# Performance work log

Hardware: AMD Instinct MI355X
Metric: run time of the kernel (lower is better)

## Reference

```python
import jax, jax.numpy as jnp
import numpy as np
from jax import lax

DN = ('NCHW', 'OIHW', 'NCHW')
N_LEVELS = 5


def conv(x, w, b=None, stride=1):
    y = lax.conv_general_dilated(x, w, (stride, stride), 'VALID', dimension_numbers=DN)
    if b is not None:
        y = y + b.reshape(1, -1, 1, 1)
    return y


def conv3_replicate(x, w, b):
    # 3x3 conv, padding=1, padding_mode='replicate'
    xp = jnp.pad(x, ((0, 0), (0, 0), (1, 1), (1, 1)), mode='edge')
    return conv(xp, w, b)


def conv_transpose3_s2(x, w):
    # ConvTranspose2d(k=3, stride=2, padding=0): n -> 2n+1
    return lax.conv_general_dilated(x, jnp.flip(w, (2, 3)), (1, 1), [(2, 2), (2, 2)],
                                    lhs_dilation=(2, 2), dimension_numbers=DN)


def setup_inputs() -> dict:
    key = jax.random.key(0)
    ks = jax.random.split(key, 12)
    B = 1024
    u = jax.random.normal(ks[0], (B, 1, 127, 127), jnp.float32)
    f = jax.random.normal(ks[1], (B, 1, 127, 127), jnp.float32)
    a = jax.random.uniform(ks[2], (B, 1, 128, 128), jnp.float32)
    s = 0.3
    c0_w = jax.random.normal(ks[3], (N_LEVELS, 1, 1, 3, 3), jnp.float32) * s  # Conv_Dyn.conv_0
    c0_b = jax.random.normal(ks[4], (N_LEVELS, 1), jnp.float32) * s
    c1_w = jax.random.normal(ks[5], (N_LEVELS, 1, 1, 2, 2), jnp.float32) * s  # Conv_Dyn.conv_1
    c1_b = jax.random.normal(ks[6], (N_LEVELS, 1), jnp.float32) * s
    r1_w = jax.random.normal(ks[7], (N_LEVELS - 1, 1, 1, 2, 2), jnp.float32) * s  # MgRestriction.R_1
    r3_w = jax.random.normal(ks[8], (N_LEVELS - 1, 1, 1, 3, 3), jnp.float32) * s  # MgRestriction.R_3
    t_w = jax.random.normal(ks[9], (N_LEVELS - 1, 1, 1, 3, 3), jnp.float32) * s  # transpose_layers
    return dict(u=u, f=f, a=a, c0_w=c0_w, c0_b=c0_b, c1_w=c1_w, c1_b=c1_b,
                r1_w=r1_w, r3_w=r3_w, t_w=t_w)


def reference(u, f, a, c0_w, c0_b, c1_w, c1_b, r1_w, r3_w, t_w):
    a_top = a
    # level 0: Conv_Dyn with u given, diva None
    diva = conv(a, c1_w[0], c1_b[0])                 # [B,1,127,127]
    r = f - diva * u
    u_lvl = u + conv3_replicate(jnp.tanh(diva), c0_w[0], c0_b[0]) * r
    diva_list = [diva]
    us = [u_lvl]
    # levels 1..4: restriction then Conv_Dyn (u=None branch, f=None so r kept)
    for i in range(1, N_LEVELS):
        a = conv(a, r1_w[i - 1], stride=2)           # R_1: k2 s2
        r = conv(r, r3_w[i - 1], stride=2)           # R_3: k3 s2
        diva = conv(a, c1_w[i], c1_b[i])
        u_lvl = conv3_replicate(jnp.tanh(diva), c0_w[i], c0_b[i]) * r
        diva_list.append(diva)
        us.append(u_lvl)
    # prolongation: coarse-to-fine residual additions
    for i in range(N_LEVELS - 2, -1, -1):
        us[i] = us[i] + conv_transpose3_s2(us[i + 1], t_w[i])
    return (us[0], f, a_top, *diva_list)
```

## Files before the change

kernel.cpp:

```cpp
#include <hip/hip_runtime.h>
#include <cmath>

#define BATCH 1024

__global__ __launch_bounds__(256) void k_L01(
    const float* __restrict__ u, const float* __restrict__ f, const float* __restrict__ a,
    const float* __restrict__ c0w, const float* __restrict__ c0b,
    const float* __restrict__ c1w, const float* __restrict__ c1b,
    const float* __restrict__ r1w, const float* __restrict__ r3w,
    float* __restrict__ out_us0, float* __restrict__ out_diva0,
    float* __restrict__ out_f, float* __restrict__ out_a,
    float* __restrict__ out_diva1,
    float* __restrict__ ws_a1, float* __restrict__ ws_r1, float* __restrict__ ws_us1)
{
    const int b = blockIdx.y;
    const int bx = blockIdx.x;
    const int Y0 = bx * 16;
    const int y0 = bx * 8;
    const int tid = threadIdx.x;

    __shared__ float asrc[22][128];
    __shared__ float td0[18][128];
    __shared__ float r0s[17][128];
    __shared__ float a1s[11][66];
    __shared__ float td1[10][64];

    const float* ab = a + (size_t)b * 16384;
    for (int i = tid; i < 22 * 128; i += 256) {
        int r = i >> 7, c = i & 127;
        int g = Y0 - 2 + r; g = g < 0 ? 0 : (g > 127 ? 127 : g);
        asrc[r][c] = ab[g * 128 + c];
    }
    __syncthreads();

    const float w00 = c1w[0], w01 = c1w[1], w10 = c1w[2], w11 = c1w[3], b1 = c1b[0];
    for (int i = tid; i < 18 * 127; i += 256) {
        int r = i / 127, c = i % 127;
        int g = Y0 - 1 + r;
        if (g >= 0 && g <= 126) {
            float d = asrc[r + 1][c] * w00 + asrc[r + 1][c + 1] * w01
                    + asrc[r + 2][c] * w10 + asrc[r + 2][c + 1] * w11 + b1;
            td0[r][c] = tanhf(d);
        }
    }
    __syncthreads();

    {
        float* oa = out_a + (size_t)b * 16384 + (size_t)Y0 * 128;
        for (int i = tid; i < 16 * 128; i += 256)
            oa[i] = asrc[(i >> 7) + 2][i & 127];
    }

    const float c0b0 = c0b[0];
    for (int i = tid; i < 17 * 127; i += 256) {
        int rr = i / 127, c = i % 127;
        int g = Y0 + rr;
        if (g > 126) continue;
        float diva = asrc[rr + 2][c] * w00 + asrc[rr + 2][c + 1] * w01
                   + asrc[rr + 3][c] * w10 + asrc[rr + 3][c + 1] * w11 + b1;
        size_t idx = (size_t)b * 16129 + (size_t)g * 127 + c;
        float uv = u[idx], fv = f[idx];
        float rv = fv - diva * uv;
        r0s[rr][c] = rv;
        if (rr < 16) {
            float s = c0b0;
            #pragma unroll
            for (int ky = 0; ky < 3; ky++) {
                int sy = g - 1 + ky; sy = sy < 0 ? 0 : (sy > 126 ? 126 : sy);
                int lr = sy - (Y0 - 1);
                #pragma unroll
                for (int kx = 0; kx < 3; kx++) {
                    int sx = c - 1 + kx; sx = sx < 0 ? 0 : (sx > 126 ? 126 : sx);
                    s += c0w[ky * 3 + kx] * td0[lr][sx];
                }
            }
            out_diva0[idx] = diva;
            out_us0[idx] = uv + s * rv;
            out_f[idx] = fv;
        }
    }

    const float q00 = r1w[0], q01 = r1w[1], q10 = r1w[2], q11 = r1w[3];
    for (int i = tid; i < 11 * 66; i += 256) {
        int rA = i / 66, cA = i % 66;
        int ay = y0 - 1 + rA; ay = ay < 0 ? 0 : (ay > 63 ? 63 : ay);
        int ax = cA - 1; ax = ax < 0 ? 0 : (ax > 63 ? 63 : ax);
        int la = 2 * ay - Y0 + 2;
        a1s[rA][cA] = asrc[la][2 * ax] * q00 + asrc[la][2 * ax + 1] * q01
                    + asrc[la + 1][2 * ax] * q10 + asrc[la + 1][2 * ax + 1] * q11;
    }
    __syncthreads();

    {
        float* a1o = ws_a1 + (size_t)b * 4096 + (size_t)y0 * 64;
        for (int i = tid; i < 8 * 64; i += 256)
            a1o[i] = a1s[(i >> 6) + 1][(i & 63) + 1];
    }

    const float v00 = c1w[4], v01 = c1w[5], v10 = c1w[6], v11 = c1w[7], b2 = c1b[1];
    for (int i = tid; i < 10 * 63; i += 256) {
        int rt = i / 63, c = i % 63;
        int dy = y0 - 1 + rt;
        if (dy >= 0 && dy <= 62) {
            float d = a1s[rt][c + 1] * v00 + a1s[rt][c + 2] * v01
                    + a1s[rt + 1][c + 1] * v10 + a1s[rt + 1][c + 2] * v11 + b2;
            td1[rt][c] = tanhf(d);
        }
    }
    __syncthreads();

    const float c0b1 = c0b[1];
    const float* c0w1 = c0w + 9;
    const float* r3 = r3w;
    for (int i = tid; i < 8 * 63; i += 256) {
        int row = i / 63, col = i % 63;
        int y = y0 + row;
        if (y > 62) continue;
        float diva = a1s[row + 1][col + 1] * v00 + a1s[row + 1][col + 2] * v01
                   + a1s[row + 2][col + 1] * v10 + a1s[row + 2][col + 2] * v11 + b2;
        float rv = 0.f;
        #pragma unroll
        for (int p = 0; p < 3; p++)
            #pragma unroll
            for (int q = 0; q < 3; q++)
                rv += r3[p * 3 + q] * r0s[2 * row + p][2 * col + q];
        float s = c0b1;
        #pragma unroll
        for (int ky = 0; ky < 3; ky++) {
            int sy = y - 1 + ky; sy = sy < 0 ? 0 : (sy > 62 ? 62 : sy);
            int lr = sy - (y0 - 1);
            #pragma unroll
            for (int kx = 0; kx < 3; kx++) {
                int sx = col - 1 + kx; sx = sx < 0 ? 0 : (sx > 62 ? 62 : sx);
                s += c0w1[ky * 3 + kx] * td1[lr][sx];
            }
        }
        size_t idx = (size_t)b * 3969 + (size_t)y * 63 + col;
        out_diva1[idx] = diva;
        ws_r1[idx] = rv;
        ws_us1[idx] = s * rv;
    }
}

template<int N, int NA, int PA, int PD>
__device__ __forceinline__ void level_step(
    const float* ap, const float* rp, float* ac, float* rc, float* us, float* td,
    const float* __restrict__ r1w, const float* __restrict__ r3w,
    const float* __restrict__ c1w, float c1b_,
    const float* __restrict__ c0w, float c0b_,
    float* __restrict__ diva_out, int tid)
{
    const float q00 = r1w[0], q01 = r1w[1], q10 = r1w[2], q11 = r1w[3];
    for (int idx = tid; idx < NA * NA; idx += 256) {
        int y = idx / NA, x = idx % NA;
        const float* p = ap + 2 * y * PA + 2 * x;
        ac[idx] = p[0] * q00 + p[1] * q01 + p[PA] * q10 + p[PA + 1] * q11;
    }
    __syncthreads();
    const float w00 = c1w[0], w01 = c1w[1], w10 = c1w[2], w11 = c1w[3];
    for (int idx = tid; idx < N * N; idx += 256) {
        int y = idx / N, x = idx % N;
        float d = ac[y * NA + x] * w00 + ac[y * NA + x + 1] * w01
                + ac[(y + 1) * NA + x] * w10 + ac[(y + 1) * NA + x + 1] * w11 + c1b_;
        td[idx] = tanhf(d);
        diva_out[idx] = d;
    }
    __syncthreads();
    for (int idx = tid; idx < N * N; idx += 256) {
        int y = idx / N, x = idx % N;
        float rv = 0.f;
        #pragma unroll
        for (int p = 0; p < 3; p++)
            #pragma unroll
            for (int q = 0; q < 3; q++)
                rv += r3w[p * 3 + q] * rp[(2 * y + p) * PD + 2 * x + q];
        float s = c0b_;
        #pragma unroll
        for (int ky = 0; ky < 3; ky++) {
            int sy = y - 1 + ky; sy = sy < 0 ? 0 : (sy > N - 1 ? N - 1 : sy);
            #pragma unroll
            for (int kx = 0; kx < 3; kx++) {
                int sx = x - 1 + kx; sx = sx < 0 ? 0 : (sx > N - 1 ? N - 1 : sx);
                s += c0w[ky * 3 + kx] * td[sy * N + sx];
            }
        }
        rc[idx] = rv;
        us[idx] = s * rv;
    }
    __syncthreads();
}

template<int NO, int NI>
__device__ __forceinline__ void prolong_step(
    float* uo, const float* ui, const float* __restrict__ tw9, int tid)
{
    for (int idx = tid; idx < NO * NO; idx += 256) {
        int y = idx / NO, x = idx % NO;
        float acc = 0.f;
        #pragma unroll
        for (int ky = 0; ky < 3; ky++) {
            int sy = y - ky;
            if (sy & 1) continue;
            int iy = sy >> 1;
            if (iy < 0 || iy >= NI) continue;
            #pragma unroll
            for (int kx = 0; kx < 3; kx++) {
                int sx = x - kx;
                if (sx & 1) continue;
                int ix = sx >> 1;
                if (ix < 0 || ix >= NI) continue;
                acc += tw9[ky * 3 + kx] * ui[iy * NI + ix];
            }
        }
        uo[idx] += acc;
    }
    __syncthreads();
}

__global__ __launch_bounds__(256) void k_coarse(
    const float* __restrict__ a1, const float* __restrict__ r1,
    const float* __restrict__ r1w, const float* __restrict__ r3w,
    const float* __restrict__ c1w, const float* __restrict__ c1b,
    const float* __restrict__ c0w, const float* __restrict__ c0b,
    const float* __restrict__ tw,
    float* __restrict__ diva2, float* __restrict__ diva3, float* __restrict__ diva4,
    float* __restrict__ us2_out)
{
    const int b = blockIdx.x;
    const int tid = threadIdx.x;
    __shared__ float aA[64 * 64];
    __shared__ float rA[63 * 63];
    __shared__ float aB[32 * 32];
    __shared__ float rB[31 * 31];
    __shared__ float aC[16 * 16];
    __shared__ float rC[15 * 15];
    __shared__ float aD[8 * 8];
    __shared__ float rD[7 * 7];
    __shared__ float us2s[31 * 31];
    __shared__ float us3s[15 * 15];
    __shared__ float us4s[7 * 7];
    __shared__ float td[31 * 31];

    const float* a1b = a1 + (size_t)b * 4096;
    const float* r1b = r1 + (size_t)b * 3969;
    for (int i = tid; i < 4096; i += 256) aA[i] = a1b[i];
    for (int i = tid; i < 3969; i += 256) rA[i] = r1b[i];
    __syncthreads();

    level_step<31, 32, 64, 63>(aA, rA, aB, rB, us2s, td,
        r1w + 4, r3w + 9, c1w + 8, c1b[2], c0w + 18, c0b[2],
        diva2 + (size_t)b * 961, tid);
    level_step<15, 16, 32, 31>(aB, rB, aC, rC, us3s, td,
        r1w + 8, r3w + 18, c1w + 12, c1b[3], c0w + 27, c0b[3],
        diva3 + (size_t)b * 225, tid);
    level_step<7, 8, 16, 15>(aC, rC, aD, rD, us4s, td,
        r1w + 12, r3w + 27, c1w + 16, c1b[4], c0w + 36, c0b[4],
        diva4 + (size_t)b * 49, tid);

    prolong_step<15, 7>(us3s, us4s, tw + 27, tid);
    prolong_step<31, 15>(us2s, us3s, tw + 18, tid);

    for (int i = tid; i < 961; i += 256)
        us2_out[(size_t)b * 961 + i] = us2s[i];
}

__global__ __launch_bounds__(256) void k_prolong2(
    float* __restrict__ us0, const float* __restrict__ us1, const float* __restrict__ us2,
    const float* __restrict__ tw)
{
    const int b = blockIdx.y;
    const int bx = blockIdx.x;
    const int Y0 = bx * 16;
    const int y0 = bx * 8;
    const int tid = threadIdx.x;
    __shared__ float us2s[6][32];
    __shared__ float us1p[9][64];

    const float* i2 = us2 + (size_t)b * 961;
    for (int i = tid; i < 6 * 31; i += 256) {
        int r = i / 31, c = i % 31;
        int jy = 4 * bx - 2 + r;
        if (jy >= 0 && jy <= 30) us2s[r][c] = i2[jy * 31 + c];
    }
    __syncthreads();

    const float* t1 = tw + 9;
    const float* i1 = us1 + (size_t)b * 3969;
    for (int i = tid; i < 9 * 63; i += 256) {
        int r = i / 63, c = i % 63;
        int iy = y0 - 1 + r;
        if (iy < 0 || iy > 62) continue;
        float acc = i1[iy * 63 + c];
        #pragma unroll
        for (int ky = 0; ky < 3; ky++) {
            int sy = iy - ky;
            if ((sy & 1) || sy < 0) continue;
            int jy = sy >> 1;
            if (jy > 30) continue;
            int lr = jy - (4 * bx - 2);
            #pragma unroll
            for (int kx = 0; kx < 3; kx++) {
                int sx = c - kx;
                if ((sx & 1) || sx < 0) continue;
                int jx = sx >> 1;
                if (jx > 30) continue;
                acc += t1[ky * 3 + kx] * us2s[lr][jx];
            }
        }
        us1p[r][c] = acc;
    }
    __syncthreads();

    const float* t0 = tw;
    float* o0 = us0 + (size_t)b * 16129;
    for (int i = tid; i < 16 * 127; i += 256) {
        int row = i / 127, col = i % 127;
        int y = Y0 + row;
        if (y > 126) continue;
        float acc = 0.f;
        #pragma unroll
        for (int ky = 0; ky < 3; ky++) {
            int sy = y - ky;
            if ((sy & 1) || sy < 0) continue;
            int iy = sy >> 1;
            if (iy > 62) continue;
            int lr = iy - (y0 - 1);
            #pragma unroll
            for (int kx = 0; kx < 3; kx++) {
                int sx = col - kx;
                if ((sx & 1) || sx < 0) continue;
                int ix = sx >> 1;
                if (ix > 62) continue;
                acc += t0[ky * 3 + kx] * us1p[lr][ix];
            }
        }
        o0[(size_t)y * 127 + col] += acc;
    }
}

extern "C" void kernel_launch(void* const* d_in, const int* in_sizes, int n_in,
                              void* d_out, int out_size, void* d_ws, size_t ws_size,
                              hipStream_t stream) {
    const float* u   = (const float*)d_in[0];
    const float* f   = (const float*)d_in[1];
    const float* a   = (const float*)d_in[2];
    const float* c0w = (const float*)d_in[3];
    const float* c0b = (const float*)d_in[4];
    const float* c1w = (const float*)d_in[5];
    const float* c1b = (const float*)d_in[6];
    const float* r1w = (const float*)d_in[7];
    const float* r3w = (const float*)d_in[8];
    const float* tw  = (const float*)d_in[9];
    float* out = (float*)d_out;
    float* ws  = (float*)d_ws;
    const size_t B = BATCH;

    size_t off_us0 = 0;
    size_t off_f   = B * 16129;
    size_t off_a   = off_f + B * 16129;
    size_t off_d0  = off_a + B * 16384;
    size_t off_d1  = off_d0 + B * 16129;
    size_t off_d2  = off_d1 + B * 3969;
    size_t off_d3  = off_d2 + B * 961;
    size_t off_d4  = off_d3 + B * 225;

    size_t w_a1  = 0;
    size_t w_r1  = w_a1 + B * 4096;
    size_t w_us1 = w_r1 + B * 3969;
    size_t w_us2 = w_us1 + B * 3969;

    dim3 blk(256);
    k_L01<<<dim3(8, B), blk, 0, stream>>>(
        u, f, a, c0w, c0b, c1w, c1b, r1w, r3w,
        out + off_us0, out + off_d0, out + off_f, out + off_a,
        out + off_d1, ws + w_a1, ws + w_r1, ws + w_us1);

    k_coarse<<<dim3(1024), blk, 0, stream>>>(
        ws + w_a1, ws + w_r1, r1w, r3w, c1w, c1b, c0w, c0b, tw,
        out + off_d2, out + off_d3, out + off_d4, ws + w_us2);

    k_prolong2<<<dim3(8, B), blk, 0, stream>>>(
        out + off_us0, ws + w_us1, ws + w_us2, tw);
}
```

Baseline: 602.1 us.

## Halve L01 tile height, use 2D thread mapping, vectorize loads, read level1 from global

The fine-level kernel now handles 8 rows per block instead of 16, doubling the grid and shrinking shared memory, and adds a launch bound asking for 8 blocks per SM to raise occupancy. Flat index loops with div/mod are replaced by 2D thread mappings, and the copy of `a` to shared memory and to the output uses float4. The restriction into a1s is moved before the first barrier, removing one sync. The coarse kernel no longer stages the 64x64 level-1 arrays in shared memory and reads them straight from global, which cuts LDS use at the cost of uncached strided global reads; the prolongation kernel gets the same 2D index rewrite.

```diff
diff --git a/kernel.cpp b/kernel.cpp
--- a/kernel.cpp
+++ b/kernel.cpp
@@ -3,7 +3,7 @@
 
 #define BATCH 1024
 
-__global__ __launch_bounds__(256) void k_L01(
+__global__ __launch_bounds__(256, 8) void k_L01(
     const float* __restrict__ u, const float* __restrict__ f, const float* __restrict__ a,
     const float* __restrict__ c0w, const float* __restrict__ c0b,
     const float* __restrict__ c1w, const float* __restrict__ c1b,
@@ -15,54 +15,73 @@
 {
     const int b = blockIdx.y;
     const int bx = blockIdx.x;
-    const int Y0 = bx * 16;
-    const int y0 = bx * 8;
+    const int Y0 = bx * 8;
+    const int y0 = bx * 4;
     const int tid = threadIdx.x;
 
-    __shared__ float asrc[22][128];
-    __shared__ float td0[18][128];
-    __shared__ float r0s[17][128];
-    __shared__ float a1s[11][66];
-    __shared__ float td1[10][64];
-
-    const float* ab = a + (size_t)b * 16384;
-    for (int i = tid; i < 22 * 128; i += 256) {
-        int r = i >> 7, c = i & 127;
-        int g = Y0 - 2 + r; g = g < 0 ? 0 : (g > 127 ? 127 : g);
-        asrc[r][c] = ab[g * 128 + c];
+    __shared__ float asrc[14][128];
+    __shared__ float td0[10][128];
+    __shared__ float r0s[9][128];
+    __shared__ float a1s[7][68];
+    __shared__ float td1[6][64];
+
+    {
+        const float4* ab4 = reinterpret_cast<const float4*>(a + (size_t)b * 16384);
+        float4* s4 = reinterpret_cast<float4*>(&asrc[0][0]);
+        const int c4 = tid & 31, r4 = tid >> 5;
+        #pragma unroll
+        for (int r = r4; r < 14; r += 8) {
+            int g = Y0 - 2 + r; g = g < 0 ? 0 : (g > 127 ? 127 : g);
+            s4[r * 32 + c4] = ab4[g * 32 + c4];
+        }
     }
     __syncthreads();
 
     const float w00 = c1w[0], w01 = c1w[1], w10 = c1w[2], w11 = c1w[3], b1 = c1b[0];
-    for (int i = tid; i < 18 * 127; i += 256) {
-        int r = i / 127, c = i % 127;
+    const int tx = tid & 127, ty = tid >> 7;
+
+    #pragma unroll
+    for (int r = ty; r < 10; r += 2) {
         int g = Y0 - 1 + r;
-        if (g >= 0 && g <= 126) {
-            float d = asrc[r + 1][c] * w00 + asrc[r + 1][c + 1] * w01
-                    + asrc[r + 2][c] * w10 + asrc[r + 2][c + 1] * w11 + b1;
-            td0[r][c] = tanhf(d);
-        }
-    }
-    __syncthreads();
-
-    {
-        float* oa = out_a + (size_t)b * 16384 + (size_t)Y0 * 128;
-        for (int i = tid; i < 16 * 128; i += 256)
-            oa[i] = asrc[(i >> 7) + 2][i & 127];
-    }
+        if (g >= 0 && g <= 126 && tx < 127) {
+            float d = asrc[r + 1][tx] * w00 + asrc[r + 1][tx + 1] * w01
+                    + asrc[r + 2][tx] * w10 + asrc[r + 2][tx + 1] * w11 + b1;
+            td0[r][tx] = tanhf(d);
+        }
+    }
+    {
+        float4* oa4 = reinterpret_cast<float4*>(out_a + (size_t)b * 16384);
+        const float4* s4 = reinterpret_cast<const float4*>(&asrc[0][0]);
+        const int c4 = tid & 31, r4 = tid >> 5;
+        oa4[(Y0 + r4) * 32 + c4] = s4[(r4 + 2) * 32 + c4];
+    }
+    const float q00 = r1w[0], q01 = r1w[1], q10 = r1w[2], q11 = r1w[3];
+    {
+        const int tx2 = tid & 63, ty2 = tid >> 6;
+        #pragma unroll
+        for (int r = ty2; r < 7; r += 4)
+            for (int c = tx2; c < 66; c += 64) {
+                int ay = y0 - 1 + r; ay = ay < 0 ? 0 : (ay > 63 ? 63 : ay);
+                int ax = c - 1; ax = ax < 0 ? 0 : (ax > 63 ? 63 : ax);
+                int la = 2 * ay - (Y0 - 2);
+                a1s[r][c] = asrc[la][2 * ax] * q00 + asrc[la][2 * ax + 1] * q01
+                          + asrc[la + 1][2 * ax] * q10 + asrc[la + 1][2 * ax + 1] * q11;
+            }
+    }
+    __syncthreads();
 
     const float c0b0 = c0b[0];
-    for (int i = tid; i < 17 * 127; i += 256) {
-        int rr = i / 127, c = i % 127;
+    #pragma unroll
+    for (int rr = ty; rr < 9; rr += 2) {
         int g = Y0 + rr;
-        if (g > 126) continue;
-        float diva = asrc[rr + 2][c] * w00 + asrc[rr + 2][c + 1] * w01
-                   + asrc[rr + 3][c] * w10 + asrc[rr + 3][c + 1] * w11 + b1;
-        size_t idx = (size_t)b * 16129 + (size_t)g * 127 + c;
+        if (g > 126 || tx >= 127) continue;
+        float diva = asrc[rr + 2][tx] * w00 + asrc[rr + 2][tx + 1] * w01
+                   + asrc[rr + 3][tx] * w10 + asrc[rr + 3][tx + 1] * w11 + b1;
+        size_t idx = (size_t)b * 16129 + (size_t)g * 127 + tx;
         float uv = u[idx], fv = f[idx];
         float rv = fv - diva * uv;
-        r0s[rr][c] = rv;
-        if (rr < 16) {
+        r0s[rr][tx] = rv;
+        if (rr < 8) {
             float s = c0b0;
             #pragma unroll
             for (int ky = 0; ky < 3; ky++) {
@@ -70,7 +89,7 @@
                 int lr = sy - (Y0 - 1);
                 #pragma unroll
                 for (int kx = 0; kx < 3; kx++) {
-                    int sx = c - 1 + kx; sx = sx < 0 ? 0 : (sx > 126 ? 126 : sx);
+                    int sx = tx - 1 + kx; sx = sx < 0 ? 0 : (sx > 126 ? 126 : sx);
                     s += c0w[ky * 3 + kx] * td0[lr][sx];
                 }
             }
@@ -80,65 +99,50 @@
         }
     }
 
-    const float q00 = r1w[0], q01 = r1w[1], q10 = r1w[2], q11 = r1w[3];
-    for (int i = tid; i < 11 * 66; i += 256) {
-        int rA = i / 66, cA = i % 66;
-        int ay = y0 - 1 + rA; ay = ay < 0 ? 0 : (ay > 63 ? 63 : ay);
-        int ax = cA - 1; ax = ax < 0 ? 0 : (ax > 63 ? 63 : ax);
-        int la = 2 * ay - Y0 + 2;
-        a1s[rA][cA] = asrc[la][2 * ax] * q00 + asrc[la][2 * ax + 1] * q01
-                    + asrc[la + 1][2 * ax] * q10 + asrc[la + 1][2 * ax + 1] * q11;
-    }
-    __syncthreads();
-
-    {
-        float* a1o = ws_a1 + (size_t)b * 4096 + (size_t)y0 * 64;
-        for (int i = tid; i < 8 * 64; i += 256)
-            a1o[i] = a1s[(i >> 6) + 1][(i & 63) + 1];
-    }
-
     const float v00 = c1w[4], v01 = c1w[5], v10 = c1w[6], v11 = c1w[7], b2 = c1b[1];
-    for (int i = tid; i < 10 * 63; i += 256) {
-        int rt = i / 63, c = i % 63;
-        int dy = y0 - 1 + rt;
-        if (dy >= 0 && dy <= 62) {
-            float d = a1s[rt][c + 1] * v00 + a1s[rt][c + 2] * v01
-                    + a1s[rt + 1][c + 1] * v10 + a1s[rt + 1][c + 2] * v11 + b2;
-            td1[rt][c] = tanhf(d);
-        }
-    }
-    __syncthreads();
-
-    const float c0b1 = c0b[1];
-    const float* c0w1 = c0w + 9;
-    const float* r3 = r3w;
-    for (int i = tid; i < 8 * 63; i += 256) {
-        int row = i / 63, col = i % 63;
-        int y = y0 + row;
-        if (y > 62) continue;
-        float diva = a1s[row + 1][col + 1] * v00 + a1s[row + 1][col + 2] * v01
-                   + a1s[row + 2][col + 1] * v10 + a1s[row + 2][col + 2] * v11 + b2;
-        float rv = 0.f;
-        #pragma unroll
-        for (int p = 0; p < 3; p++)
-            #pragma unroll
-            for (int q = 0; q < 3; q++)
-                rv += r3[p * 3 + q] * r0s[2 * row + p][2 * col + q];
-        float s = c0b1;
-        #pragma unroll
-        for (int ky = 0; ky < 3; ky++) {
-            int sy = y - 1 + ky; sy = sy < 0 ? 0 : (sy > 62 ? 62 : sy);
-            int lr = sy - (y0 - 1);
-            #pragma unroll
-            for (int kx = 0; kx < 3; kx++) {
-                int sx = col - 1 + kx; sx = sx < 0 ? 0 : (sx > 62 ? 62 : sx);
-                s += c0w1[ky * 3 + kx] * td1[lr][sx];
-            }
-        }
-        size_t idx = (size_t)b * 3969 + (size_t)y * 63 + col;
-        out_diva1[idx] = diva;
-        ws_r1[idx] = rv;
-        ws_us1[idx] = s * rv;
+    {
+        const int tx2 = tid & 63, ty2 = tid >> 6;
+        ws_a1[(size_t)b * 4096 + (size_t)(y0 + ty2) * 64 + tx2] = a1s[ty2 + 1][tx2 + 1];
+        #pragma unroll
+        for (int r = ty2; r < 6; r += 4) {
+            int dy = y0 - 1 + r;
+            if (dy >= 0 && dy <= 62 && tx2 < 63) {
+                float d = a1s[r][tx2 + 1] * v00 + a1s[r][tx2 + 2] * v01
+                        + a1s[r + 1][tx2 + 1] * v10 + a1s[r + 1][tx2 + 2] * v11 + b2;
+                td1[r][tx2] = tanhf(d);
+            }
+        }
+    }
+    __syncthreads();
+
+    {
+        const int tx2 = tid & 63, ty2 = tid >> 6;
+        const int y = y0 + ty2;
+        if (y <= 62 && tx2 < 63) {
+            float diva = a1s[ty2 + 1][tx2 + 1] * v00 + a1s[ty2 + 1][tx2 + 2] * v01
+                       + a1s[ty2 + 2][tx2 + 1] * v10 + a1s[ty2 + 2][tx2 + 2] * v11 + b2;
+            float rv = 0.f;
+            #pragma unroll
+            for (int p = 0; p < 3; p++)
+                #pragma unroll
+                for (int q = 0; q < 3; q++)
+                    rv += r3w[p * 3 + q] * r0s[2 * ty2 + p][2 * tx2 + q];
+            float s = c0b[1];
+            #pragma unroll
+            for (int ky = 0; ky < 3; ky++) {
+                int sy = y - 1 + ky; sy = sy < 0 ? 0 : (sy > 62 ? 62 : sy);
+                int lr = sy - (y0 - 1);
+                #pragma unroll
+                for (int kx = 0; kx < 3; kx++) {
+                    int sx = tx2 - 1 + kx; sx = sx < 0 ? 0 : (sx > 62 ? 62 : sx);
+                    s += c0w[9 + ky * 3 + kx] * td1[lr][sx];
+                }
+            }
+            size_t idx = (size_t)b * 3969 + (size_t)y * 63 + tx2;
+            out_diva1[idx] = diva;
+            ws_r1[idx] = rv;
+            ws_us1[idx] = s * rv;
+        }
     }
 }
 
@@ -228,8 +232,6 @@
 {
     const int b = blockIdx.x;
     const int tid = threadIdx.x;
-    __shared__ float aA[64 * 64];
-    __shared__ float rA[63 * 63];
     __shared__ float aB[32 * 32];
     __shared__ float rB[31 * 31];
     __shared__ float aC[16 * 16];
@@ -241,13 +243,8 @@
     __shared__ float us4s[7 * 7];
     __shared__ float td[31 * 31];
 
-    const float* a1b = a1 + (size_t)b * 4096;
-    const float* r1b = r1 + (size_t)b * 3969;
-    for (int i = tid; i < 4096; i += 256) aA[i] = a1b[i];
-    for (int i = tid; i < 3969; i += 256) rA[i] = r1b[i];
-    __syncthreads();
-
-    level_step<31, 32, 64, 63>(aA, rA, aB, rB, us2s, td,
+    level_step<31, 32, 64, 63>(a1 + (size_t)b * 4096, r1 + (size_t)b * 3969,
+        aB, rB, us2s, td,
         r1w + 4, r3w + 9, c1w + 8, c1b[2], c0w + 18, c0b[2],
         diva2 + (size_t)b * 961, tid);
     level_step<15, 16, 32, 31>(aB, rB, aC, rC, us3s, td,
@@ -276,65 +273,73 @@
     __shared__ float us2s[6][32];
     __shared__ float us1p[9][64];
 
-    const float* i2 = us2 + (size_t)b * 961;
-    for (int i = tid; i < 6 * 31; i += 256) {
-        int r = i / 31, c = i % 31;
-        int jy = 4 * bx - 2 + r;
-        if (jy >= 0 && jy <= 30) us2s[r][c] = i2[jy * 31 + c];
+    {
+        const float* i2 = us2 + (size_t)b * 961;
+        const int tx3 = tid & 31, ty3 = tid >> 5;
+        if (ty3 < 6 && tx3 < 31) {
+            int jy = 4 * bx - 2 + ty3;
+            if (jy >= 0 && jy <= 30) us2s[ty3][tx3] = i2[jy * 31 + tx3];
+        }
     }
     __syncthreads();
 
     const float* t1 = tw + 9;
-    const float* i1 = us1 + (size_t)b * 3969;
-    for (int i = tid; i < 9 * 63; i += 256) {
-        int r = i / 63, c = i % 63;
-        int iy = y0 - 1 + r;
-        if (iy < 0 || iy > 62) continue;
-        float acc = i1[iy * 63 + c];
-        #pragma unroll
-        for (int ky = 0; ky < 3; ky++) {
-            int sy = iy - ky;
-            if ((sy & 1) || sy < 0) continue;
-            int jy = sy >> 1;
-            if (jy > 30) continue;
-            int lr = jy - (4 * bx - 2);
-            #pragma unroll
-            for (int kx = 0; kx < 3; kx++) {
-                int sx = c - kx;
-                if ((sx & 1) || sx < 0) continue;
-                int jx = sx >> 1;
-                if (jx > 30) continue;
-                acc += t1[ky * 3 + kx] * us2s[lr][jx];
-            }
-        }
-        us1p[r][c] = acc;
+    {
+        const float* i1 = us1 + (size_t)b * 3969;
+        const int tx2 = tid & 63, ty2 = tid >> 6;
+        #pragma unroll
+        for (int r = ty2; r < 9; r += 4) {
+            int iy = y0 - 1 + r;
+            if (iy < 0 || iy > 62 || tx2 >= 63) continue;
+            float acc = i1[iy * 63 + tx2];
+            #pragma unroll
+            for (int ky = 0; ky < 3; ky++) {
+                int sy = iy - ky;
+                if ((sy & 1) || sy < 0) continue;
+                int jy = sy >> 1;
+                if (jy > 30) continue;
+                int lr = jy - (4 * bx - 2);
+                #pragma unroll
+                for (int kx = 0; kx < 3; kx++) {
+                    int sx = tx2 - kx;
+                    if ((sx & 1) || sx < 0) continue;
+                    int jx = sx >> 1;
+                    if (jx > 30) continue;
+                    acc += t1[ky * 3 + kx] * us2s[lr][jx];
+                }
+            }
+            us1p[r][tx2] = acc;
+        }
     }
     __syncthreads();
 
     const float* t0 = tw;
-    float* o0 = us0 + (size_t)b * 16129;
-    for (int i = tid; i < 16 * 127; i += 256) {
-        int row = i / 127, col = i % 127;
-        int y = Y0 + row;
-        if (y > 126) continue;
-        float acc = 0.f;
-        #pragma unroll
-        for (int ky = 0; ky < 3; ky++) {
-            int sy = y - ky;
-            if ((sy & 1) || sy < 0) continue;
-            int iy = sy >> 1;
-            if (iy > 62) continue;
-            int lr = iy - (y0 - 1);
-            #pragma unroll
-            for (int kx = 0; kx < 3; kx++) {
-                int sx = col - kx;
-                if ((sx & 1) || sx < 0) continue;
-                int ix = sx >> 1;
-                if (ix > 62) continue;
-                acc += t0[ky * 3 + kx] * us1p[lr][ix];
-            }
-        }
-        o0[(size_t)y * 127 + col] += acc;
+    {
+        float* o0 = us0 + (size_t)b * 16129;
+        const int tx = tid & 127, ty = tid >> 7;
+        #pragma unroll
+        for (int row = ty; row < 16; row += 2) {
+            int y = Y0 + row;
+            if (y > 126 || tx >= 127) continue;
+            float acc = 0.f;
+            #pragma unroll
+            for (int ky = 0; ky < 3; ky++) {
+                int sy = y - ky;
+                if ((sy & 1) || sy < 0) continue;
+                int iy = sy >> 1;
+                if (iy > 62) continue;
+                int lr = iy - (y0 - 1);
+                #pragma unroll
+                for (int kx = 0; kx < 3; kx++) {
+                    int sx = tx - kx;
+                    if ((sx & 1) || sx < 0) continue;
+                    int ix = sx >> 1;
+                    if (ix > 62) continue;
+                    acc += t0[ky * 3 + kx] * us1p[lr][ix];
+                }
+            }
+            o0[(size_t)y * 127 + tx] += acc;
+        }
     }
 }
 
@@ -370,7 +375,7 @@
     size_t w_us2 = w_us1 + B * 3969;
 
     dim3 blk(256);
-    k_L01<<<dim3(8, B), blk, 0, stream>>>(
+    k_L01<<<dim3(16, B), blk, 0, stream>>>(
         u, f, a, c0w, c0b, c1w, c1b, r1w, r3w,
         out + off_us0, out + off_d0, out + off_f, out + off_a,
         out + off_d1, ws + w_a1, ws + w_r1, ws + w_us1);
```

Result: faster. 511.0 us (-15.1%).
